# Kernel tuning notes

Measured on AMD Instinct MI355X. Metric: run time of the kernel, lower is better.

Reference implementation:

```python
import jax, jax.numpy as jnp
import numpy as np

N = 51200      # total nodes
E = 1638400    # total edges (avg degree 32)
G = 512        # graphs in batch
IN = 16        # input node features
H = 4          # heads
C = 32         # channels per head
HC = H * C     # 128, concat output width
SLOPE = 0.2    # LeakyReLU negative slope
BN_EPS = 1e-5


def _glorot(k, shape, fan):
    return jax.random.normal(k, shape, jnp.float32) / np.sqrt(fan).astype(np.float32)


def setup_inputs() -> dict:
    key = jax.random.key(0)
    ks = jax.random.split(key, 32)
    inp = {}
    inp['x'] = jax.random.normal(ks[0], (N, IN), jnp.float32)
    inp['edge_index'] = jax.random.randint(ks[1], (2, E), 0, N)
    inp['batch'] = jnp.sort(jax.random.randint(ks[2], (N,), 0, G))
    # GATv2 layer 1 (IN -> H*C)
    inp['l1_Wl'] = _glorot(ks[3], (IN, HC), IN)
    inp['l1_bl'] = jnp.zeros((HC,), jnp.float32)
    inp['l1_Wr'] = _glorot(ks[4], (IN, HC), IN)
    inp['l1_br'] = jnp.zeros((HC,), jnp.float32)
    inp['l1_att'] = _glorot(ks[5], (H, C), C)
    inp['l1_bias'] = jnp.zeros((HC,), jnp.float32)
    # GATv2 layer 2 (HC -> H*C)
    inp['l2_Wl'] = _glorot(ks[6], (HC, HC), HC)
    inp['l2_bl'] = jnp.zeros((HC,), jnp.float32)
    inp['l2_Wr'] = _glorot(ks[7], (HC, HC), HC)
    inp['l2_br'] = jnp.zeros((HC,), jnp.float32)
    inp['l2_att'] = _glorot(ks[8], (H, C), C)
    inp['l2_bias'] = jnp.zeros((HC,), jnp.float32)
    # MLP head (HC -> HC -> HC -> 2) with BatchNorm (eval mode, running stats 0/1)
    inp['fc1_W'] = _glorot(ks[9], (HC, HC), HC)
    inp['fc1_b'] = jnp.zeros((HC,), jnp.float32)
    inp['bn1_g'] = jnp.ones((HC,), jnp.float32)
    inp['bn1_b'] = jnp.zeros((HC,), jnp.float32)
    inp['fc2_W'] = _glorot(ks[10], (HC, HC), HC)
    inp['fc2_b'] = jnp.zeros((HC,), jnp.float32)
    inp['bn2_g'] = jnp.ones((HC,), jnp.float32)
    inp['bn2_b'] = jnp.zeros((HC,), jnp.float32)
    inp['fc3_W'] = _glorot(ks[11], (HC, 2), HC)
    inp['fc3_b'] = jnp.zeros((2,), jnp.float32)
    return inp


def gatv2_conv(x, src, dst, Wl, bl, Wr, br, att, bias):
    # PyG GATv2Conv (share_weights=False, concat=True), eval mode (no dropout).
    xl = (x @ Wl + bl).reshape(-1, H, C)  # source transform  [N,H,C]
    xr = (x @ Wr + br).reshape(-1, H, C)  # target transform  [N,H,C]
    e = jax.nn.leaky_relu(xl[src] + xr[dst], SLOPE)   # [E,H,C]
    score = jnp.einsum('ehc,hc->eh', e, att)          # [E,H]
    # segment softmax over edges sharing the same target node
    m = jax.ops.segment_max(score, dst, num_segments=N)
    ex = jnp.exp(score - m[dst])
    denom = jax.ops.segment_sum(ex, dst, num_segments=N)
    alpha = ex / (denom[dst] + 1e-16)                 # [E,H]
    out = jax.ops.segment_sum(xl[src] * alpha[:, :, None], dst, num_segments=N)
    return out.reshape(-1, HC) + bias


def reference(x, edge_index, batch,
              l1_Wl, l1_bl, l1_Wr, l1_br, l1_att, l1_bias,
              l2_Wl, l2_bl, l2_Wr, l2_br, l2_att, l2_bias,
              fc1_W, fc1_b, bn1_g, bn1_b,
              fc2_W, fc2_b, bn2_g, bn2_b,
              fc3_W, fc3_b):
    src, dst = edge_index[0], edge_index[1]
    h = jax.nn.relu(gatv2_conv(x, src, dst, l1_Wl, l1_bl, l1_Wr, l1_br, l1_att, l1_bias))
    h = jax.nn.relu(gatv2_conv(h, src, dst, l2_Wl, l2_bl, l2_Wr, l2_br, l2_att, l2_bias))
    # global mean pool over graphs
    s = jax.ops.segment_sum(h, batch, num_segments=G)
    cnt = jax.ops.segment_sum(jnp.ones((N,), h.dtype), batch, num_segments=G)
    g = s / jnp.maximum(cnt, 1.0)[:, None]            # [G,HC]
    # MLP head; BatchNorm1d in eval mode with running_mean=0, running_var=1
    def bn(z, gamma, beta):
        return z * (gamma / np.sqrt(1.0 + BN_EPS).astype(np.float32)) + beta
    g = jax.nn.relu(bn(g @ fc1_W + fc1_b, bn1_g, bn1_b))
    g = jax.nn.relu(bn(g @ fc2_W + fc2_b, bn2_g, bn2_b))
    return g @ fc3_W + fc3_b                          # [G,2]
```

## Files before the change

### kernel.cpp

```cpp
#include <hip/hip_runtime.h>
#include <math.h>

#define NN 51200
#define EE 1638400
#define GG 512
#define INF 16
#define HCC 128
#define NB 400
#define TILE 4096
#define CSRCAP 4608
#define NBLK8 (NN / 8)

typedef float vf2 __attribute__((ext_vector_type(2)));
typedef short v8s __attribute__((ext_vector_type(8)));
typedef float v4f __attribute__((ext_vector_type(4)));
typedef _Float16 vh8 __attribute__((ext_vector_type(8)));
typedef float vf8 __attribute__((ext_vector_type(8)));
#define FMA2 __builtin_elementwise_fma
#define MIN2 __builtin_elementwise_min
#define MAX2 __builtin_elementwise_max


__device__ __forceinline__ int wave_incl_scan(int v, int lane) {
#pragma unroll
    for (int d = 1; d < 64; d <<= 1) {
        int y = __shfl_up(v, d);
        if (lane >= d) v += y;
    }
    return v;
}

__device__ __forceinline__ unsigned short bf16_rtne(float f) {
    unsigned u = __builtin_bit_cast(unsigned, f);
    unsigned r = u + 0x7FFFu + ((u >> 16) & 1u);
    return (unsigned short)(r >> 16);
}

__device__ __forceinline__ unsigned short f16_rtne(float f) {
    return __builtin_bit_cast(unsigned short, (_Float16)f);
}

__device__ __forceinline__ float dpp_xor1(float x) {
    int y = __builtin_amdgcn_mov_dpp(__builtin_bit_cast(int, x), 0xB1, 0xF, 0xF, true);
    return __builtin_bit_cast(float, y);
}
__device__ __forceinline__ float dpp_xor2(float x) {
    int y = __builtin_amdgcn_mov_dpp(__builtin_bit_cast(int, x), 0x4E, 0xF, 0xF, true);
    return __builtin_bit_cast(float, y);
}
__device__ __forceinline__ float dpp_xor8(float x) {
    int y = __builtin_amdgcn_mov_dpp(__builtin_bit_cast(int, x), 0x128, 0xF, 0xF, true);
    return __builtin_bit_cast(float, y);
}

__global__ __launch_bounds__(512) void k_hist(const int* __restrict__ ei,
                                              int* __restrict__ bcnt) {
    __shared__ int h[NB];
    int t = threadIdx.x;
    if (t < NB) h[t] = 0;
    __syncthreads();
    int e0 = blockIdx.x * TILE;
#pragma unroll
    for (int s = 0; s < 8; s++) {
        int d = ei[EE + e0 + s * 512 + t];
        atomicAdd(&h[d >> 7], 1);
    }
    __syncthreads();
    if (t < NB && h[t]) atomicAdd(&bcnt[t], h[t]);
}

__global__ __launch_bounds__(512) void k_scan2(const int* __restrict__ bcnt,
                                               int* __restrict__ bbase,
                                               int* __restrict__ gcur,
                                               int* __restrict__ rowptr) {
    __shared__ int sc[512];
    int t = threadIdx.x;
    int v = (t < NB) ? bcnt[t] : 0;
    sc[t] = v;
    __syncthreads();
    for (int off = 1; off < 512; off <<= 1) {
        int u = (t >= off) ? sc[t - off] : 0;
        __syncthreads();
        sc[t] += u;
        __syncthreads();
    }
    if (t < NB) { int ex = sc[t] - v; bbase[t] = ex; gcur[t] = ex; }
    if (t == 0) { bbase[NB] = EE; rowptr[NN] = EE; }
}

__global__ __launch_bounds__(512) void k_binlin1(const int* __restrict__ ei,
                                                 int* __restrict__ gcur,
                                                 unsigned* __restrict__ binned,
                                                 const float* __restrict__ x,
                                                 const float* __restrict__ Wl,
                                                 const float* __restrict__ bl,
                                                 const float* __restrict__ Wr,
                                                 const float* __restrict__ br,
                                                 unsigned short* __restrict__ xl,
                                                 float* __restrict__ xr,
                                                 const float* __restrict__ W2l,
                                                 const float* __restrict__ W2r,
                                                 unsigned short* __restrict__ Bhi,
                                                 unsigned short* __restrict__ Blo,
                                                 const int* __restrict__ batch,
                                                 int* __restrict__ gbound) {
    __shared__ int h[512];
    __shared__ int lexcl[NB], lcur[NB], baseg[NB];
    __shared__ unsigned stage[TILE];
    __shared__ int wsum[8];
    __shared__ float sx[16][INF];
    int t = threadIdx.x;
    if (blockIdx.x < NB) {
        int lane = t & 63, w = t >> 6;
        h[t] = 0;
        __syncthreads();
        int e0 = blockIdx.x * TILE;
        int sv[8], dv[8];
#pragma unroll
        for (int s = 0; s < 8; s++) {
            int e = e0 + s * 512 + t;
            sv[s] = ei[e];
            dv[s] = ei[EE + e];
            atomicAdd(&h[dv[s] >> 7], 1);
        }
        __syncthreads();
        int myh = h[t];
        int incl = wave_incl_scan(myh, lane);
        if (lane == 63) wsum[w] = incl;
        __syncthreads();
        int woff = 0;
        for (int i = 0; i < w; i++) woff += wsum[i];
        incl += woff;
        if (t < NB) {
            int ex = incl - myh;
            lexcl[t] = ex;
            lcur[t] = ex;
            baseg[t] = atomicAdd(&gcur[t], myh);
        }
        __syncthreads();
#pragma unroll
        for (int s = 0; s < 8; s++) {
            int b = dv[s] >> 7;
            int r = atomicAdd(&lcur[b], 1);
            stage[r] = (unsigned)sv[s] | ((unsigned)dv[s] << 16);
        }
        __syncthreads();
#pragma unroll
        for (int s = 0; s < 8; s++) {
            int idx = s * 512 + t;
            unsigned p = stage[idx];
            int b = (int)(p >> 23);
            binned[baseg[b] + idx - lexcl[b]] = p;
        }
    } else if (blockIdx.x < NB + NN / 16) {
        int bid = blockIdx.x - NB;
        int j = t & 127;
        int ty = t >> 7;
        if (t < 256) {
            sx[t >> 4][t & 15] = x[(size_t)(bid * 16 + (t >> 4)) * INF + (t & 15)];
        }
        __syncthreads();
#pragma unroll
        for (int it = 0; it < 4; it++) {
            int rl = it * 4 + ty;
            int row = bid * 16 + rl;
            float al = bl[j], ar = br[j];
#pragma unroll
            for (int k = 0; k < INF; k++) {
                float xv = sx[rl][k];
                al = fmaf(xv, Wl[k * HCC + j], al);
                ar = fmaf(xv, Wr[k * HCC + j], ar);
            }
            int head = j >> 5, ch = j & 31;
            xl[((size_t)(head >> 1) * NN + row) * 64 + (head & 1) * 32 + ch] = f16_rtne(al);
            xr[((size_t)head * NN + row) * 32 + ch] = ar;
        }
    } else if (blockIdx.x < NB + NN / 16 + 8) {
        int gt = (blockIdx.x - NB - NN / 16) * 512 + t;
        int ks = gt >> 10;
        int rem = gt & 1023;
        int nt = rem >> 6;
        int lane = rem & 63;
        int n = nt * 16 + (lane & 15);
        int kbase = ks * 32 + (lane >> 4) * 8;
        const float* src = (n < 128) ? (W2l + n) : (W2r + n - 128);
        unsigned short hi8[8], lo8[8];
#pragma unroll
        for (int j = 0; j < 8; j++) {
            float v = src[(size_t)(kbase + j) * HCC];
            unsigned short hb = bf16_rtne(v);
            float hf = __builtin_bit_cast(float, (unsigned)hb << 16);
            hi8[j] = hb;
            lo8[j] = bf16_rtne(v - hf);
        }
        size_t idx = (size_t)gt * 8;
#pragma unroll
        for (int j = 0; j < 8; j++) { Bhi[idx + j] = hi8[j]; Blo[idx + j] = lo8[j]; }
    } else {
        int n = (blockIdx.x - NB - NN / 16 - 8) * 512 + t;
        int bn = batch[n];
        int bp = (n == 0) ? -1 : batch[n - 1];
        for (int g = bp + 1; g <= bn; g++) gbound[g] = n;
        if (n == NN - 1) {
            for (int g = bn + 1; g <= GG; g++) gbound[g] = NN;
        }
    }
}

__global__ __launch_bounds__(512) void k_csr(const unsigned* __restrict__ binned,
                                             const int* __restrict__ bbase,
                                             int* __restrict__ rowptr,
                                             int* __restrict__ col) {
    int b = blockIdx.x;
    int base = bbase[b];
    int cnt = bbase[b + 1] - base;
    __shared__ int nh[1024], ncur[1024];
    __shared__ unsigned sbin[CSRCAP];
    __shared__ int wsum[8];
    int t = threadIdx.x;
    int lane = t & 63, w = t >> 6;
    nh[t] = 0;
    nh[t + 512] = 0;
    __syncthreads();
    for (int e = t; e < cnt; e += 512) {
        unsigned p = binned[base + e];
        if (e < CSRCAP) sbin[e] = p;
        unsigned src = p & 0xFFFFu;
        int key = (int)(((p >> 16) & 127u) << 3) | (int)(src >> 13);
        atomicAdd(&nh[key], 1);
    }
    __syncthreads();
    int c0 = nh[2 * t], c1 = nh[2 * t + 1];
    int tot = c0 + c1;
    int incl = wave_incl_scan(tot, lane);
    if (lane == 63) wsum[w] = incl;
    __syncthreads();
    int woff = 0;
    for (int i = 0; i < w; i++) woff += wsum[i];
    int tex = incl + woff - tot;
    ncur[2 * t] = base + tex;
    ncur[2 * t + 1] = base + tex + c0;
    if ((t & 3) == 0) rowptr[(b << 7) + (t >> 2)] = base + tex;
    __syncthreads();
    for (int e = t; e < cnt; e += 512) {
        unsigned p = (e < CSRCAP) ? sbin[e] : binned[base + e];
        unsigned src = p & 0xFFFFu;
        int key = (int)(((p >> 16) & 127u) << 3) | (int)(src >> 13);
        int r = atomicAdd(&ncur[key], 1);
        col[r] = (int)src;
    }
}

__global__ __launch_bounds__(256) void k_lin2(const float* __restrict__ hin,
                                              const unsigned short* __restrict__ Bhi,
                                              const unsigned short* __restrict__ Blo,
                                              const float* __restrict__ bl,
                                              const float* __restrict__ br,
                                              unsigned short* __restrict__ outl,
                                              float* __restrict__ outr) {
    const int tid = threadIdx.x;
    const int wv = tid >> 6;
    const int lane = tid & 63;
    const int m = lane & 15;
    const int quad = lane >> 4;
    const int r0 = blockIdx.x * 64 + wv * 16;
    const float* arow = hin + (size_t)(r0 + m) * HCC + quad * 8;
    const v8s* bh = (const v8s*)Bhi;
    const v8s* bo = (const v8s*)Blo;

    v4f acc[16];
#pragma unroll
    for (int nt = 0; nt < 16; nt++) acc[nt] = (v4f){0.f, 0.f, 0.f, 0.f};

#pragma unroll
    for (int ks = 0; ks < 4; ks++) {
        const float4 av0 = *(const float4*)(arow + ks * 32);
        const float4 av1 = *(const float4*)(arow + ks * 32 + 4);
        const float af[8] = {av0.x, av0.y, av0.z, av0.w, av1.x, av1.y, av1.z, av1.w};
        v8s ahi, alo;
#pragma unroll
        for (int e = 0; e < 8; e++) {
            unsigned short hb = bf16_rtne(af[e]);
            float hf = __builtin_bit_cast(float, (unsigned)hb << 16);
            ahi[e] = (short)hb;
            alo[e] = (short)bf16_rtne(af[e] - hf);
        }
        const int base = ks * 16 * 64 + lane;
#pragma unroll
        for (int nt = 0; nt < 16; nt++) {
            v8s bhv = bh[base + nt * 64];
            v8s blv = bo[base + nt * 64];
            acc[nt] = __builtin_amdgcn_mfma_f32_16x16x32_bf16(ahi, bhv, acc[nt], 0, 0, 0);
            acc[nt] = __builtin_amdgcn_mfma_f32_16x16x32_bf16(ahi, blv, acc[nt], 0, 0, 0);
            acc[nt] = __builtin_amdgcn_mfma_f32_16x16x32_bf16(alo, bhv, acc[nt], 0, 0, 0);
        }
    }
#pragma unroll
    for (int nt = 0; nt < 16; nt++) {
        int n = nt * 16 + m;
        int c = n & 127;
        float bv = (n < 128) ? bl[c] : br[c];
        if (n < 128) {
            int head = c >> 5, ch = c & 31;
            unsigned short* op = outl + (size_t)(head >> 1) * NN * 64 + (head & 1) * 32 + ch;
#pragma unroll
            for (int r = 0; r < 4; r++) {
                int row = r0 + quad * 4 + r;
                op[(size_t)row * 64] = f16_rtne(acc[nt][r] + bv);
            }
        } else {
            float* op = outr + (size_t)(c >> 5) * NN * 32 + (c & 31);
#pragma unroll
            for (int r = 0; r < 4; r++) {
                int row = r0 + quad * 4 + r;
                op[(size_t)row * 32] = acc[nt][r] + bv;
            }
        }
    }
}

__global__ __launch_bounds__(512) void k_attn(const int* __restrict__ rowptr,
                                              const int* __restrict__ col,
                                              const unsigned short* __restrict__ xl,
                                              const float* __restrict__ xr,
                                              const float* __restrict__ att,
                                              const float* __restrict__ bias,
                                              float* __restrict__ hout) {
    const int wave = threadIdx.x >> 6;
    const int lane = threadIdx.x & 63;
    const int sub = lane >> 3;
    const int hl = (lane >> 2) & 1;
    const int hq = lane & 3;
    const int pair = blockIdx.x / NBLK8;
    const int n = (blockIdx.x - pair * NBLK8) * 8 + wave;
    const int head = 2 * pair + hl;

    const char* xlq = (const char*)(xl + (size_t)pair * NN * 64)
                      + (unsigned)(hl * 64 + hq * 16);
    const float* xrp = xr + ((size_t)head * NN + n) * 32 + hq * 8;
    const float4 xrv0 = *(const float4*)(xrp);
    const float4 xrv1 = *(const float4*)(xrp + 4);
    const float4 at0 = *(const float4*)(att + head * 32 + hq * 8);
    const float4 at1 = *(const float4*)(att + head * 32 + hq * 8 + 4);
    const float LOG2E = 1.44269504088896340736f;
    const vf2 xr01 = {xrv0.x, xrv0.y}, xr23 = {xrv0.z, xrv0.w};
    const vf2 xr45 = {xrv1.x, xrv1.y}, xr67 = {xrv1.z, xrv1.w};
    const vf2 at01 = {at0.x * LOG2E, at0.y * LOG2E}, at23 = {at0.z * LOG2E, at0.w * LOG2E};
    const vf2 at45 = {at1.x * LOG2E, at1.y * LOG2E}, at67 = {at1.z * LOG2E, at1.w * LOG2E};
    const vf2 Z2 = {0.f, 0.f}, C2 = {0.2f, 0.2f};

    const int base = rowptr[n];
    const int deg = rowptr[n + 1] - base;

    float l = 0.f;
    vf2 a01 = Z2, a23 = Z2, a45 = Z2, a67 = Z2;

    for (int i0 = 0; i0 < deg; i0 += 64) {
        int mye = 0;
        if (i0 + lane < deg) mye = col[base + i0 + lane];
        const int cnt = min(64, deg - i0);
        const int events = (cnt + 15) >> 4;
        vh8 ca, cb, na{}, nb{};
        {
            const int s0 = __shfl(mye, sub);
            const int s1 = __shfl(mye, 8 + sub);
            ca = *(const vh8*)(xlq + (((unsigned)s0) << 7));
            cb = *(const vh8*)(xlq + (((unsigned)s1) << 7));
        }
        for (int g = 0; g < events; ++g) {
            if (g + 1 < events) {
                const int s0 = __shfl(mye, 16 * (g + 1) + sub);
                const int s1 = __shfl(mye, 16 * (g + 1) + 8 + sub);
                na = *(const vh8*)(xlq + (((unsigned)s0) << 7));
                nb = *(const vh8*)(xlq + (((unsigned)s1) << 7));
            }
#pragma unroll
            for (int k = 0; k < 2; ++k) {
                const vf8 fv = __builtin_convertvector(k ? cb : ca, vf8);
                const vf2 v01 = {fv[0], fv[1]}, v23 = {fv[2], fv[3]};
                const vf2 v45 = {fv[4], fv[5]}, v67 = {fv[6], fv[7]};
                vf2 e, kk, p2;
                e = v01 + xr01; kk = FMA2(C2, MIN2(e, Z2), MAX2(e, Z2)); p2 = kk * at01;
                e = v23 + xr23; kk = FMA2(C2, MIN2(e, Z2), MAX2(e, Z2)); p2 = FMA2(kk, at23, p2);
                e = v45 + xr45; kk = FMA2(C2, MIN2(e, Z2), MAX2(e, Z2)); p2 = FMA2(kk, at45, p2);
                e = v67 + xr67; kk = FMA2(C2, MIN2(e, Z2), MAX2(e, Z2)); p2 = FMA2(kk, at67, p2);
                float pp = p2.x + p2.y;
                pp += dpp_xor1(pp);
                pp += dpp_xor2(pp);
                if ((16 * g + 8 * k + sub) >= cnt) pp = -INFINITY;
                const float w = __builtin_amdgcn_exp2f(pp);
                l += w;
                const vf2 W = {w, w};
                a01 = FMA2(W, v01, a01);
                a23 = FMA2(W, v23, a23);
                a45 = FMA2(W, v45, a45);
                a67 = FMA2(W, v67, a67);
            }
            ca = na;
            cb = nb;
        }
    }
    l += dpp_xor8(l);
    l += __shfl_xor(l, 16);
    l += __shfl_xor(l, 32);
    float af[8] = {a01.x, a01.y, a23.x, a23.y, a45.x, a45.y, a67.x, a67.y};
#pragma unroll
    for (int i = 0; i < 8; i++) {
        af[i] += dpp_xor8(af[i]);
        af[i] += __shfl_xor(af[i], 16);
        af[i] += __shfl_xor(af[i], 32);
    }
    const float inv = 1.f / (l + 1e-16f);
    if (sub == 0) {
        const float4 b0 = *(const float4*)(bias + head * 32 + hq * 8);
        const float4 b1 = *(const float4*)(bias + head * 32 + hq * 8 + 4);
        float4 o0, o1;
        o0.x = fmaxf(fmaf(af[0], inv, b0.x), 0.f);
        o0.y = fmaxf(fmaf(af[1], inv, b0.y), 0.f);
        o0.z = fmaxf(fmaf(af[2], inv, b0.z), 0.f);
        o0.w = fmaxf(fmaf(af[3], inv, b0.w), 0.f);
        o1.x = fmaxf(fmaf(af[4], inv, b1.x), 0.f);
        o1.y = fmaxf(fmaf(af[5], inv, b1.y), 0.f);
        o1.z = fmaxf(fmaf(af[6], inv, b1.z), 0.f);
        o1.w = fmaxf(fmaf(af[7], inv, b1.w), 0.f);
        float* hp = hout + (size_t)n * HCC + head * 32 + hq * 8;
        *(float4*)(hp) = o0;
        *(float4*)(hp + 4) = o1;
    }
}

__global__ __launch_bounds__(128) void k_head(const float* __restrict__ h,
                                              const int* __restrict__ gbound,
                                              const float* __restrict__ fc1W, const float* __restrict__ fc1b,
                                              const float* __restrict__ bn1g, const float* __restrict__ bn1b,
                                              const float* __restrict__ fc2W, const float* __restrict__ fc2b,
                                              const float* __restrict__ bn2g, const float* __restrict__ bn2b,
                                              const float* __restrict__ fc3W, const float* __restrict__ fc3b,
                                              float* __restrict__ out) {
    int g = blockIdx.x;
    int j = threadIdx.x;
    __shared__ float buf[HCC], buf2[HCC];
    int s = gbound[g];
    int e = gbound[g + 1];
    float s0 = 0.f, s1 = 0.f, s2 = 0.f, s3 = 0.f;
    int n = s;
    for (; n + 3 < e; n += 4) {
        s0 += h[(size_t)n * HCC + j];
        s1 += h[(size_t)(n + 1) * HCC + j];
        s2 += h[(size_t)(n + 2) * HCC + j];
        s3 += h[(size_t)(n + 3) * HCC + j];
    }
    for (; n < e; n++) s0 += h[(size_t)n * HCC + j];
    float sum = (s0 + s1) + (s2 + s3);
    float cnt = (float)(e - s);
    buf[j] = sum / fmaxf(cnt, 1.0f);
    __syncthreads();
    const float SQ = 1.00000499998749994f;
    float a = fc1b[j];
    for (int k = 0; k < HCC; k++) a = fmaf(buf[k], fc1W[k * HCC + j], a);
    a = fmaf(a, bn1g[j] / SQ, bn1b[j]);
    a = fmaxf(a, 0.f);
    buf2[j] = a;
    __syncthreads();
    a = fc2b[j];
    for (int k = 0; k < HCC; k++) a = fmaf(buf2[k], fc2W[k * HCC + j], a);
    a = fmaf(a, bn2g[j] / SQ, bn2b[j]);
    a = fmaxf(a, 0.f);
    buf[j] = a;
    __syncthreads();
    if (j < 2) {
        float o = fc3b[j];
        for (int k = 0; k < HCC; k++) o = fmaf(buf[k], fc3W[k * 2 + j], o);
        out[g * 2 + j] = o;
    }
}

extern "C" void kernel_launch(void* const* d_in, const int* in_sizes, int n_in,
                              void* d_out, int out_size, void* d_ws, size_t ws_size,
                              hipStream_t stream) {
    const float* x      = (const float*)d_in[0];
    const int*   ei     = (const int*)d_in[1];
    const int*   batch  = (const int*)d_in[2];
    const float* l1_Wl  = (const float*)d_in[3];
    const float* l1_bl  = (const float*)d_in[4];
    const float* l1_Wr  = (const float*)d_in[5];
    const float* l1_br  = (const float*)d_in[6];
    const float* l1_att = (const float*)d_in[7];
    const float* l1_bias= (const float*)d_in[8];
    const float* l2_Wl  = (const float*)d_in[9];
    const float* l2_bl  = (const float*)d_in[10];
    const float* l2_Wr  = (const float*)d_in[11];
    const float* l2_br  = (const float*)d_in[12];
    const float* l2_att = (const float*)d_in[13];
    const float* l2_bias= (const float*)d_in[14];
    const float* fc1_W  = (const float*)d_in[15];
    const float* fc1_b  = (const float*)d_in[16];
    const float* bn1_g  = (const float*)d_in[17];
    const float* bn1_b  = (const float*)d_in[18];
    const float* fc2_W  = (const float*)d_in[19];
    const float* fc2_b  = (const float*)d_in[20];
    const float* bn2_g  = (const float*)d_in[21];
    const float* bn2_b  = (const float*)d_in[22];
    const float* fc3_W  = (const float*)d_in[23];
    const float* fc3_b  = (const float*)d_in[24];
    float* out = (float*)d_out;

    unsigned short* xlh = (unsigned short*)d_ws;
    float* xr = (float*)(xlh + (size_t)NN * HCC);
    float* h  = xr + (size_t)NN * HCC;
    int* rowptr = (int*)(h + (size_t)NN * HCC);
    int* col    = rowptr + (NN + 1);
    int* bcnt   = col + EE;
    int* bbase  = bcnt + NB;
    int* gcur   = bbase + (NB + 1);
    int* gbound = gcur + NB;
    uintptr_t bp = ((uintptr_t)(gbound + GG + 1) + 15) & ~(uintptr_t)15;
    unsigned short* Bhi = (unsigned short*)bp;
    unsigned short* Blo = Bhi + 32768;
    unsigned* binned = (unsigned*)h;

    hipMemsetAsync(bcnt, 0, NB * sizeof(int), stream);
    k_hist<<<EE / TILE, 512, 0, stream>>>(ei, bcnt);
    k_scan2<<<1, 512, 0, stream>>>(bcnt, bbase, gcur, rowptr);
    k_binlin1<<<NB + NN / 16 + 8 + NN / 512, 512, 0, stream>>>(
        ei, gcur, binned, x, l1_Wl, l1_bl, l1_Wr, l1_br, xlh, xr,
        l2_Wl, l2_Wr, Bhi, Blo, batch, gbound);
    k_csr<<<NB, 512, 0, stream>>>(binned, bbase, rowptr, col);

    k_attn<<<2 * NBLK8, 512, 0, stream>>>(rowptr, col, xlh, xr, l1_att, l1_bias, h);

    k_lin2<<<NN / 64, 256, 0, stream>>>(h, Bhi, Blo, l2_bl, l2_br, xlh, xr);
    k_attn<<<2 * NBLK8, 512, 0, stream>>>(rowptr, col, xlh, xr, l2_att, l2_bias, h);

    k_head<<<GG, 128, 0, stream>>>(h, gbound, fc1_W, fc1_b, bn1_g, bn1_b,
                                   fc2_W, fc2_b, bn2_g, bn2_b, fc3_W, fc3_b, out);
}
```

Measured before the change: 417.4 us.

## Use nontemporal loads/stores, vectorize edge-index reads, split head pooling across two groups

Edge-index reads in the histogram and binning kernels now use 16-byte vector loads instead of scalar loads. Many streaming global loads and stores across the lin, CSR, attention and lin2 kernels become nontemporal. The head kernel doubles its threads so that two groups each pool half the node rows. The nontemporal hints may hurt where data such as xr, col and h is reused across kernels through the cache, and the vector loads change which edges each thread handles.

```diff
diff --git a/kernel.cpp b/kernel.cpp
--- a/kernel.cpp
+++ b/kernel.cpp
@@ -14,11 +14,13 @@
 typedef float vf2 __attribute__((ext_vector_type(2)));
 typedef short v8s __attribute__((ext_vector_type(8)));
 typedef float v4f __attribute__((ext_vector_type(4)));
+typedef int v4i __attribute__((ext_vector_type(4)));
 typedef _Float16 vh8 __attribute__((ext_vector_type(8)));
 typedef float vf8 __attribute__((ext_vector_type(8)));
 #define FMA2 __builtin_elementwise_fma
 #define MIN2 __builtin_elementwise_min
 #define MAX2 __builtin_elementwise_max
+#define NTL(p) __builtin_nontemporal_load(p)
 
 
 __device__ __forceinline__ int wave_incl_scan(int v, int lane) {
@@ -59,11 +61,14 @@
     int t = threadIdx.x;
     if (t < NB) h[t] = 0;
     __syncthreads();
-    int e0 = blockIdx.x * TILE;
-#pragma unroll
-    for (int s = 0; s < 8; s++) {
-        int d = ei[EE + e0 + s * 512 + t];
-        atomicAdd(&h[d >> 7], 1);
+    const v4i* d4 = (const v4i*)(ei + EE + blockIdx.x * TILE);
+#pragma unroll
+    for (int s = 0; s < 2; s++) {
+        v4i d = NTL(&d4[s * 512 + t]);
+        atomicAdd(&h[d.x >> 7], 1);
+        atomicAdd(&h[d.y >> 7], 1);
+        atomicAdd(&h[d.z >> 7], 1);
+        atomicAdd(&h[d.w >> 7], 1);
     }
     __syncthreads();
     if (t < NB && h[t]) atomicAdd(&bcnt[t], h[t]);
@@ -115,13 +120,21 @@
         h[t] = 0;
         __syncthreads();
         int e0 = blockIdx.x * TILE;
+        const v4i* s4 = (const v4i*)(ei + e0);
+        const v4i* d4 = (const v4i*)(ei + EE + e0);
         int sv[8], dv[8];
 #pragma unroll
-        for (int s = 0; s < 8; s++) {
-            int e = e0 + s * 512 + t;
-            sv[s] = ei[e];
-            dv[s] = ei[EE + e];
-            atomicAdd(&h[dv[s] >> 7], 1);
+        for (int q = 0; q < 2; q++) {
+            v4i svv = NTL(&s4[q * 512 + t]);
+            v4i dvv = NTL(&d4[q * 512 + t]);
+            sv[q * 4 + 0] = svv.x; sv[q * 4 + 1] = svv.y;
+            sv[q * 4 + 2] = svv.z; sv[q * 4 + 3] = svv.w;
+            dv[q * 4 + 0] = dvv.x; dv[q * 4 + 1] = dvv.y;
+            dv[q * 4 + 2] = dvv.z; dv[q * 4 + 3] = dvv.w;
+            atomicAdd(&h[dvv.x >> 7], 1);
+            atomicAdd(&h[dvv.y >> 7], 1);
+            atomicAdd(&h[dvv.z >> 7], 1);
+            atomicAdd(&h[dvv.w >> 7], 1);
         }
         __syncthreads();
         int myh = h[t];
@@ -157,7 +170,7 @@
         int j = t & 127;
         int ty = t >> 7;
         if (t < 256) {
-            sx[t >> 4][t & 15] = x[(size_t)(bid * 16 + (t >> 4)) * INF + (t & 15)];
+            sx[t >> 4][t & 15] = NTL(&x[(size_t)(bid * 16 + (t >> 4)) * INF + (t & 15)]);
         }
         __syncthreads();
 #pragma unroll
@@ -223,7 +236,7 @@
     nh[t + 512] = 0;
     __syncthreads();
     for (int e = t; e < cnt; e += 512) {
-        unsigned p = binned[base + e];
+        unsigned p = NTL(&binned[base + e]);
         if (e < CSRCAP) sbin[e] = p;
         unsigned src = p & 0xFFFFu;
         int key = (int)(((p >> 16) & 127u) << 3) | (int)(src >> 13);
@@ -243,7 +256,7 @@
     if ((t & 3) == 0) rowptr[(b << 7) + (t >> 2)] = base + tex;
     __syncthreads();
     for (int e = t; e < cnt; e += 512) {
-        unsigned p = (e < CSRCAP) ? sbin[e] : binned[base + e];
+        unsigned p = (e < CSRCAP) ? sbin[e] : NTL(&binned[base + e]);
         unsigned src = p & 0xFFFFu;
         int key = (int)(((p >> 16) & 127u) << 3) | (int)(src >> 13);
         int r = atomicAdd(&ncur[key], 1);
@@ -274,8 +287,8 @@
 
 #pragma unroll
     for (int ks = 0; ks < 4; ks++) {
-        const float4 av0 = *(const float4*)(arow + ks * 32);
-        const float4 av1 = *(const float4*)(arow + ks * 32 + 4);
+        const v4f av0 = NTL((const v4f*)(arow + ks * 32));
+        const v4f av1 = NTL((const v4f*)(arow + ks * 32 + 4));
         const float af[8] = {av0.x, av0.y, av0.z, av0.w, av1.x, av1.y, av1.z, av1.w};
         v8s ahi, alo;
 #pragma unroll
@@ -313,7 +326,7 @@
 #pragma unroll
             for (int r = 0; r < 4; r++) {
                 int row = r0 + quad * 4 + r;
-                op[(size_t)row * 32] = acc[nt][r] + bv;
+                __builtin_nontemporal_store(acc[nt][r] + bv, &op[(size_t)row * 32]);
             }
         }
     }
@@ -338,8 +351,8 @@
     const char* xlq = (const char*)(xl + (size_t)pair * NN * 64)
                       + (unsigned)(hl * 64 + hq * 16);
     const float* xrp = xr + ((size_t)head * NN + n) * 32 + hq * 8;
-    const float4 xrv0 = *(const float4*)(xrp);
-    const float4 xrv1 = *(const float4*)(xrp + 4);
+    const v4f xrv0 = NTL((const v4f*)(xrp));
+    const v4f xrv1 = NTL((const v4f*)(xrp + 4));
     const float4 at0 = *(const float4*)(att + head * 32 + hq * 8);
     const float4 at1 = *(const float4*)(att + head * 32 + hq * 8 + 4);
     const float LOG2E = 1.44269504088896340736f;
@@ -357,7 +370,7 @@
 
     for (int i0 = 0; i0 < deg; i0 += 64) {
         int mye = 0;
-        if (i0 + lane < deg) mye = col[base + i0 + lane];
+        if (i0 + lane < deg) mye = NTL(&col[base + i0 + lane]);
         const int cnt = min(64, deg - i0);
         const int events = (cnt + 15) >> 4;
         vh8 ca, cb, na{}, nb{};
@@ -414,7 +427,7 @@
     if (sub == 0) {
         const float4 b0 = *(const float4*)(bias + head * 32 + hq * 8);
         const float4 b1 = *(const float4*)(bias + head * 32 + hq * 8 + 4);
-        float4 o0, o1;
+        v4f o0, o1;
         o0.x = fmaxf(fmaf(af[0], inv, b0.x), 0.f);
         o0.y = fmaxf(fmaf(af[1], inv, b0.y), 0.f);
         o0.z = fmaxf(fmaf(af[2], inv, b0.z), 0.f);
@@ -424,12 +437,12 @@
         o1.z = fmaxf(fmaf(af[6], inv, b1.z), 0.f);
         o1.w = fmaxf(fmaf(af[7], inv, b1.w), 0.f);
         float* hp = hout + (size_t)n * HCC + head * 32 + hq * 8;
-        *(float4*)(hp) = o0;
-        *(float4*)(hp + 4) = o1;
-    }
-}
-
-__global__ __launch_bounds__(128) void k_head(const float* __restrict__ h,
+        __builtin_nontemporal_store(o0, (v4f*)(hp));
+        __builtin_nontemporal_store(o1, (v4f*)(hp + 4));
+    }
+}
+
+__global__ __launch_bounds__(256) void k_head(const float* __restrict__ h,
                                               const int* __restrict__ gbound,
                                               const float* __restrict__ fc1W, const float* __restrict__ fc1b,
                                               const float* __restrict__ bn1g, const float* __restrict__ bn1b,
@@ -438,40 +451,48 @@
                                               const float* __restrict__ fc3W, const float* __restrict__ fc3b,
                                               float* __restrict__ out) {
     int g = blockIdx.x;
-    int j = threadIdx.x;
-    __shared__ float buf[HCC], buf2[HCC];
+    int t = threadIdx.x;
+    int j = t & 127;
+    int grp = t >> 7;
+    __shared__ float buf[HCC], buf2[HCC], part[2][HCC];
     int s = gbound[g];
     int e = gbound[g + 1];
-    float s0 = 0.f, s1 = 0.f, s2 = 0.f, s3 = 0.f;
-    int n = s;
-    for (; n + 3 < e; n += 4) {
-        s0 += h[(size_t)n * HCC + j];
-        s1 += h[(size_t)(n + 1) * HCC + j];
-        s2 += h[(size_t)(n + 2) * HCC + j];
-        s3 += h[(size_t)(n + 3) * HCC + j];
-    }
-    for (; n < e; n++) s0 += h[(size_t)n * HCC + j];
-    float sum = (s0 + s1) + (s2 + s3);
+    float p0 = 0.f, p1 = 0.f;
+    int n0 = s;
+    for (int n = s; n + 3 < e; n += 4) {
+        p0 += NTL(&h[(size_t)(n + 2 * grp) * HCC + j]);
+        p1 += NTL(&h[(size_t)(n + 2 * grp + 1) * HCC + j]);
+        n0 = n + 4;
+    }
+    if (grp == 0) {
+        for (int n = n0; n < e; n++) p0 += NTL(&h[(size_t)n * HCC + j]);
+    }
+    part[grp][j] = p0 + p1;
+    __syncthreads();
     float cnt = (float)(e - s);
-    buf[j] = sum / fmaxf(cnt, 1.0f);
+    if (grp == 0) buf[j] = (part[0][j] + part[1][j]) / fmaxf(cnt, 1.0f);
     __syncthreads();
     const float SQ = 1.00000499998749994f;
-    float a = fc1b[j];
-    for (int k = 0; k < HCC; k++) a = fmaf(buf[k], fc1W[k * HCC + j], a);
-    a = fmaf(a, bn1g[j] / SQ, bn1b[j]);
-    a = fmaxf(a, 0.f);
-    buf2[j] = a;
-    __syncthreads();
-    a = fc2b[j];
-    for (int k = 0; k < HCC; k++) a = fmaf(buf2[k], fc2W[k * HCC + j], a);
-    a = fmaf(a, bn2g[j] / SQ, bn2b[j]);
-    a = fmaxf(a, 0.f);
-    buf[j] = a;
-    __syncthreads();
-    if (j < 2) {
-        float o = fc3b[j];
-        for (int k = 0; k < HCC; k++) o = fmaf(buf[k], fc3W[k * 2 + j], o);
-        out[g * 2 + j] = o;
+    if (grp == 0) {
+        float a = fc1b[j];
+        for (int k = 0; k < HCC; k++) a = fmaf(buf[k], fc1W[k * HCC + j], a);
+        a = fmaf(a, bn1g[j] / SQ, bn1b[j]);
+        a = fmaxf(a, 0.f);
+        buf2[j] = a;
+    }
+    __syncthreads();
+    if (grp == 0) {
+        float a = fc2b[j];
+        for (int k = 0; k < HCC; k++) a = fmaf(buf2[k], fc2W[k * HCC + j], a);
+        a = fmaf(a, bn2g[j] / SQ, bn2b[j]);
+        a = fmaxf(a, 0.f);
+        buf[j] = a;
+    }
+    __syncthreads();
+    if (t < 2) {
+        float o = fc3b[t];
+        for (int k = 0; k < HCC; k++) o = fmaf(buf[k], fc3W[k * 2 + t], o);
+        out[g * 2 + t] = o;
     }
 }
 
@@ -532,6 +553,6 @@
     k_lin2<<<NN / 64, 256, 0, stream>>>(h, Bhi, Blo, l2_bl, l2_br, xlh, xr);
     k_attn<<<2 * NBLK8, 512, 0, stream>>>(rowptr, col, xlh, xr, l2_att, l2_bias, h);
 
-    k_head<<<GG, 128, 0, stream>>>(h, gbound, fc1_W, fc1_b, bn1_g, bn1_b,
+    k_head<<<GG, 256, 0, stream>>>(h, gbound, fc1_W, fc1_b, bn1_g, bn1_b,
                                    fc2_W, fc2_b, bn2_g, bn2_b, fc3_W, fc3_b, out);
 }
```

Result: slower. 448.4 us (+7.4%).
